# Performance work log

Measured on AMD Instinct MI355X. Metric: run time of the kernel, lower is better.

The kernel has to match this reference:

```python
import jax, jax.numpy as jnp
import numpy as np

B, D, H = 512, 1024, 2048          # batch, context_dim, l_hidden
MAX_STEPS = 8                       # config.max_l_steps
ATOL = 0.01                         # config.l_conv_atol
THR = 0.1                           # config.commitment_threshold


def setup_inputs() -> dict:
    key = jax.random.key(0)
    ks = jax.random.split(key, 20)
    mat = lambda k, shp, fi: jax.random.normal(k, shp, jnp.float32) / np.float32(np.sqrt(fi))
    inp = dict(
        enc=jax.random.normal(ks[0], (B, D), jnp.float32),
        static_context=jax.random.normal(ks[1], (B, D), jnp.float32),
        # fresh RWKV state: channel 3 (pp, running max-exponent) = -1e30
        l_state=jnp.zeros((B, H, 5), jnp.float32).at[:, :, 3].set(-1e30),
        initial_drift=0.1 * jax.random.normal(ks[2], (B, D), jnp.float32),
        # l_input_proj: Linear(2*D -> H)
        Win=mat(ks[3], (2 * D, H), 2 * D), b_in=jnp.zeros((H,), jnp.float32),
        # context_drift_proj: Linear(H -> D, bias=False)
        Wdrift=mat(ks[4], (H, D), H),
        # l_to_out: Linear(H -> D)
        Wout=mat(ks[5], (H, D), H), b_out=jnp.zeros((D,), jnp.float32),
        # RWKV cell (v4-style) parameters over hidden dim H
        mix_k=jax.random.uniform(ks[6], (H,), jnp.float32),
        mix_v=jax.random.uniform(ks[7], (H,), jnp.float32),
        mix_r=jax.random.uniform(ks[8], (H,), jnp.float32),
        mix_k2=jax.random.uniform(ks[9], (H,), jnp.float32),
        mix_r2=jax.random.uniform(ks[10], (H,), jnp.float32),
        time_decay=0.5 * jax.random.normal(ks[11], (H,), jnp.float32),
        time_first=0.5 * jax.random.normal(ks[12], (H,), jnp.float32),
        Wk=mat(ks[13], (H, H), H), Wv=mat(ks[14], (H, H), H),
        Wr=mat(ks[15], (H, H), H), Wo=mat(ks[16], (H, H), H),
        Wk2=mat(ks[17], (H, H), H), Wv2=mat(ks[18], (H, H), H),
        Wr2=mat(ks[19], (H, H), H),
    )
    return inp


def _forward(enc, static_context, l_state, initial_drift, Win, b_in, Wdrift, Wout, b_out,
             mix_k, mix_v, mix_r, mix_k2, mix_r2, time_decay, time_first,
             Wk, Wv, Wr, Wo, Wk2, Wv2, Wr2):
    def cell(x, state):
        # RWKV-style linear-attention cell. state: [B,H,5] = (x_prev_tm, aa, bb, pp, x_prev_cm)
        xx, aa, bb, pp, cc = (state[..., i] for i in range(5))
        xk = x * mix_k + xx * (1.0 - mix_k)
        xv = x * mix_v + xx * (1.0 - mix_v)
        xr = x * mix_r + xx * (1.0 - mix_r)
        r = jax.nn.sigmoid(xr @ Wr)
        k = xk @ Wk
        v = xv @ Wv
        ww = time_first + k
        q = jnp.maximum(pp, ww)
        e1 = jnp.exp(pp - q); e2 = jnp.exp(ww - q)
        wkv = (e1 * aa + e2 * v) / (e1 * bb + e2)
        ww2 = pp - jnp.exp(time_decay)
        q2 = jnp.maximum(ww2, k)
        e1b = jnp.exp(ww2 - q2); e2b = jnp.exp(k - q2)
        tm_out = (r * wkv) @ Wo
        # channel-mix half of the cell (state channel 4)
        xk2 = x * mix_k2 + cc * (1.0 - mix_k2)
        xr2 = x * mix_r2 + cc * (1.0 - mix_r2)
        r2 = jax.nn.sigmoid(xr2 @ Wr2)
        kk = jnp.square(jax.nn.relu(xk2 @ Wk2))
        out = tm_out + r2 * (kk @ Wv2)
        new_state = jnp.stack([x, e1b * aa + e2b * v, e1b * bb + e2b, q2, x], axis=-1)
        return out, new_state

    def l_input_of(drift):
        v = jnp.concatenate([enc, static_context + drift], axis=-1) @ Win + b_in
        return jnp.clip(v, -50.0, 50.0)

    def step(carry, _):
        drift, sstate, done, csum, cnt = carry
        li = l_input_of(drift)
        out, ns = cell(li, sstate)
        ns = jnp.clip(ns, -50.0, 50.0)
        delta = jnp.tanh(out @ Wdrift)
        nd = jnp.clip(drift + delta, -5.0, 5.0)
        hinge = jnp.minimum(jax.nn.relu(jnp.mean(jnp.sum(nd * nd, axis=-1)) - THR), 100.0)
        conv = jnp.mean(jnp.abs(delta)) < ATOL
        # freeze all updates once converged (early-exit semantics under jit)
        drift = jnp.where(done, drift, nd)
        sstate = jnp.where(done, sstate, ns)
        csum = jnp.where(done, csum, csum + hinge)
        cnt = jnp.where(done, cnt, cnt + 1.0)
        done = jnp.logical_or(done, conv)
        return (drift, sstate, done, csum, cnt), None

    carry0 = (initial_drift, l_state, jnp.array(False), jnp.float32(0.0), jnp.float32(0.0))
    (drift, _, _, csum, cnt), _ = jax.lax.scan(step, carry0, None, length=MAX_STEPS)

    # final commit step uses the ORIGINAL l_state (not the shadow state)
    li = l_input_of(drift)
    final_out, next_state = cell(li, l_state)
    next_state = jnp.clip(next_state, -50.0, 50.0)
    final_enc = enc + final_out @ Wout + b_out
    commitment = csum / jnp.maximum(cnt, 1.0)
    return final_enc, next_state, commitment, drift


def reference(enc, static_context, l_state, initial_drift, Win, b_in, Wdrift, Wout, b_out,
              mix_k, mix_v, mix_r, mix_k2, mix_r2, time_decay, time_first,
              Wk, Wv, Wr, Wo, Wk2, Wv2, Wr2):
    return _forward(enc, static_context, l_state, initial_drift, Win, b_in, Wdrift, Wout, b_out,
                    mix_k, mix_v, mix_r, mix_k2, mix_r2, time_decay, time_first,
                    Wk, Wv, Wr, Wo, Wk2, Wv2, Wr2)
```

## Files before the change

### kernel.cpp

```cpp
#include <hip/hip_runtime.h>
#include <hip/hip_bf16.h>

#define Bb 512
#define Dd 1024
#define Hh 2048
#define BH_ (Bb*Hh)
#define BD_ (Bb*Dd)

typedef unsigned short u16;
typedef __attribute__((ext_vector_type(8))) short short8;
typedef __attribute__((ext_vector_type(4))) float f32x4;

enum { M_F32 = 0, M_IN, M_SIG, M_SQRELU, M_OUT, M_DRIFT, M_FINAL };

struct GemmP {
    const u16* A[3];
    const u16* W[3];
    void* dst[3];
    int mode[3];
    int M, N, K;
    const int* done;
    const float* bias;
    const float* mk; const float* mv; const float* mr; const float* mk2v; const float* mr2v;
    const float* xx; const float* cc;
    const float* lstate;
    float* liF;
    float* stateOut;
    u16 *o1, *o2, *o3, *o4, *o5;
    const float* f1; const float* f2;
    float* drift; float* accAbs; float* accSq;
    const float* enc; const float* bout; float* dout;
};

__global__ __launch_bounds__(256) void gemm64(GemmP p) {
    if (p.done && *(volatile const int*)p.done) return;
    const int z = blockIdx.z;
    const u16* __restrict__ A = p.A[z];
    const u16* __restrict__ W = p.W[z];
    const int Kd = p.K;
    const int m0 = blockIdx.y * 64, n0 = blockIdx.x * 64;

    __shared__ alignas(16) u16 As[64 * 72];
    __shared__ alignas(16) u16 Bs[64 * 72];

    const int t = threadIdx.x;
    const int l = t & 63, w = t >> 6;
    const int lane16 = l & 15, quad = l >> 4;
    const int wm = w & 1, wn = w >> 1;
    const int srow = t >> 3, scol = (t & 7) * 8;

    f32x4 zero = {0.f, 0.f, 0.f, 0.f};
    f32x4 acc[2][2];
    acc[0][0] = zero; acc[0][1] = zero; acc[1][0] = zero; acc[1][1] = zero;

    const u16* a0p = A + (size_t)(m0 + srow) * Kd + scol;
    const u16* a1p = A + (size_t)(m0 + srow + 32) * Kd + scol;
    const u16* b0p = W + (size_t)(n0 + srow) * Kd + scol;
    const u16* b1p = W + (size_t)(n0 + srow + 32) * Kd + scol;

    uint4 ra0 = *(const uint4*)(const void*)a0p;
    uint4 ra1 = *(const uint4*)(const void*)a1p;
    uint4 rb0 = *(const uint4*)(const void*)b0p;
    uint4 rb1 = *(const uint4*)(const void*)b1p;

    for (int k0 = 0; k0 < Kd; k0 += 64) {
        *(uint4*)(void*)&As[srow * 72 + scol] = ra0;
        *(uint4*)(void*)&As[(srow + 32) * 72 + scol] = ra1;
        *(uint4*)(void*)&Bs[srow * 72 + scol] = rb0;
        *(uint4*)(void*)&Bs[(srow + 32) * 72 + scol] = rb1;
        __syncthreads();
        if (k0 + 64 < Kd) {
            ra0 = *(const uint4*)(const void*)(a0p + k0 + 64);
            ra1 = *(const uint4*)(const void*)(a1p + k0 + 64);
            rb0 = *(const uint4*)(const void*)(b0p + k0 + 64);
            rb1 = *(const uint4*)(const void*)(b1p + k0 + 64);
        }
#pragma unroll
        for (int kc = 0; kc < 64; kc += 32) {
            short8 a0 = *(const short8*)(const void*)&As[(wm * 32 + lane16) * 72 + kc + quad * 8];
            short8 a1 = *(const short8*)(const void*)&As[(wm * 32 + 16 + lane16) * 72 + kc + quad * 8];
            short8 b0 = *(const short8*)(const void*)&Bs[(wn * 32 + lane16) * 72 + kc + quad * 8];
            short8 b1 = *(const short8*)(const void*)&Bs[(wn * 32 + 16 + lane16) * 72 + kc + quad * 8];
            acc[0][0] = __builtin_amdgcn_mfma_f32_16x16x32_bf16(a0, b0, acc[0][0], 0, 0, 0);
            acc[0][1] = __builtin_amdgcn_mfma_f32_16x16x32_bf16(a0, b1, acc[0][1], 0, 0, 0);
            acc[1][0] = __builtin_amdgcn_mfma_f32_16x16x32_bf16(a1, b0, acc[1][0], 0, 0, 0);
            acc[1][1] = __builtin_amdgcn_mfma_f32_16x16x32_bf16(a1, b1, acc[1][1], 0, 0, 0);
        }
        __syncthreads();
    }

    const int mode = p.mode[z];
    float sabs = 0.f, ssq = 0.f;
#pragma unroll
    for (int sm = 0; sm < 2; ++sm)
#pragma unroll
        for (int sn = 0; sn < 2; ++sn)
#pragma unroll
            for (int i = 0; i < 4; ++i) {
                const int m = m0 + wm * 32 + sm * 16 + quad * 4 + i;
                const int n = n0 + wn * 32 + sn * 16 + lane16;
                const size_t idx = (size_t)m * p.N + n;
                const float v = acc[sm][sn][i];
                if (mode == M_F32) {
                    ((float*)p.dst[z])[idx] = v;
                } else if (mode == M_IN) {
                    float li = fminf(fmaxf(v + p.bias[n], -50.f), 50.f);
                    float xxv, ccv;
                    if (p.lstate) { xxv = p.lstate[idx * 5 + 0]; ccv = p.lstate[idx * 5 + 4]; }
                    else { xxv = p.xx[idx]; ccv = p.cc[idx]; }
                    float mk = p.mk[n], mv = p.mv[n], mr = p.mr[n], mk2 = p.mk2v[n], mr2 = p.mr2v[n];
                    ((__hip_bfloat16*)p.o1)[idx] = __float2bfloat16(li * mk + xxv * (1.f - mk));
                    ((__hip_bfloat16*)p.o2)[idx] = __float2bfloat16(li * mv + xxv * (1.f - mv));
                    ((__hip_bfloat16*)p.o3)[idx] = __float2bfloat16(li * mr + xxv * (1.f - mr));
                    ((__hip_bfloat16*)p.o4)[idx] = __float2bfloat16(li * mk2 + ccv * (1.f - mk2));
                    ((__hip_bfloat16*)p.o5)[idx] = __float2bfloat16(li * mr2 + ccv * (1.f - mr2));
                    if (p.lstate) { p.stateOut[idx * 5 + 0] = li; p.stateOut[idx * 5 + 4] = li; }
                    else p.liF[idx] = li;
                } else if (mode == M_SIG) {
                    ((float*)p.dst[z])[idx] = 1.f / (1.f + __expf(-v));
                } else if (mode == M_SQRELU) {
                    float r = fmaxf(v, 0.f);
                    ((__hip_bfloat16*)p.dst[z])[idx] = __float2bfloat16(r * r);
                } else if (mode == M_OUT) {
                    ((__hip_bfloat16*)p.dst[z])[idx] = __float2bfloat16(p.f1[idx] + p.f2[idx] * v);
                } else if (mode == M_DRIFT) {
                    float d = tanhf(v);
                    float nd = fminf(fmaxf(p.drift[idx] + d, -5.f), 5.f);
                    p.drift[idx] = nd;
                    sabs += fabsf(d);
                    ssq += nd * nd;
                } else {
                    p.dout[idx] = p.enc[idx] + v + p.bout[n];
                }
            }
    if (mode == M_DRIFT) {
#pragma unroll
        for (int off = 32; off > 0; off >>= 1) {
            sabs += __shfl_down(sabs, off, 64);
            ssq += __shfl_down(ssq, off, 64);
        }
        if (l == 0) { atomicAdd(p.accAbs, sabs); atomicAdd(p.accSq, ssq); }
    }
}

__global__ void transposeW(const float* __restrict__ src, u16* __restrict__ dst, int K, int N) {
    __shared__ float tile[32][33];
    int kt = blockIdx.y * 32, nt = blockIdx.x * 32;
    int tx = threadIdx.x, ty = threadIdx.y;
#pragma unroll
    for (int j = 0; j < 4; j++)
        tile[ty + j * 8][tx] = src[(size_t)(kt + ty + j * 8) * N + nt + tx];
    __syncthreads();
    __hip_bfloat16* d = (__hip_bfloat16*)dst;
#pragma unroll
    for (int j = 0; j < 4; j++)
        d[(size_t)(nt + ty + j * 8) * K + kt + tx] = __float2bfloat16(tile[tx][ty + j * 8]);
}

__global__ void initstate(const float* __restrict__ lstate, const float* __restrict__ idrift,
                          float* xx, float* aa, float* bb, float* pp, float* cc,
                          float* drift, float* scal) {
    int i = blockIdx.x * 256 + threadIdx.x;
    if (i < BH_) {
        const float* s = lstate + (size_t)i * 5;
        xx[i] = s[0]; aa[i] = s[1]; bb[i] = s[2]; pp[i] = s[3]; cc[i] = s[4];
    }
    if (i < BD_) drift[i] = idrift[i];
    if (i == 0) { ((int*)scal)[0] = 0; scal[1] = 0.f; scal[2] = 0.f; scal[3] = 0.f; scal[4] = 0.f; }
}

__global__ void prep(const float* __restrict__ enc, const float* __restrict__ sc,
                     const float* __restrict__ drift, u16* __restrict__ Acat, const int* done) {
    if (done && *(volatile const int*)done) return;
    int i = blockIdx.x * 256 + threadIdx.x;
    if (i >= BD_) return;
    int m = i >> 10, d = i & 1023;
    __hip_bfloat16* Ab = (__hip_bfloat16*)Acat;
    Ab[(size_t)m * 2048 + d] = __float2bfloat16(enc[i]);
    Ab[(size_t)m * 2048 + 1024 + d] = __float2bfloat16(sc[i] + drift[i]);
}

__global__ void mix1(const float* __restrict__ Kp, const float* __restrict__ Vp,
                     const float* __restrict__ Rp,
                     float* aa, float* bb, float* pp, float* xx, float* cc,
                     const float* __restrict__ Li,
                     const float* __restrict__ tf, const float* __restrict__ td,
                     u16* __restrict__ rwkv,
                     const float* __restrict__ lstate, float* stateOut,
                     const int* done) {
    if (done && *(volatile const int*)done) return;
    int i = blockIdx.x * 256 + threadIdx.x;
    if (i >= BH_) return;
    int h = i & (Hh - 1);
    float k = Kp[i], v = Vp[i], rpre = Rp[i];
    float a, b, P;
    if (lstate) { a = lstate[(size_t)i * 5 + 1]; b = lstate[(size_t)i * 5 + 2]; P = lstate[(size_t)i * 5 + 3]; }
    else { a = aa[i]; b = bb[i]; P = pp[i]; }
    float r = 1.f / (1.f + __expf(-rpre));
    float ww = tf[h] + k;
    float q = fmaxf(P, ww);
    float e1 = __expf(P - q), e2 = __expf(ww - q);
    float wkv = (e1 * a + e2 * v) / (e1 * b + e2);
    ((__hip_bfloat16*)rwkv)[i] = __float2bfloat16(r * wkv);
    float ww2 = P - __expf(td[h]);
    float q2 = fmaxf(ww2, k);
    float e1b = __expf(ww2 - q2), e2b = __expf(k - q2);
    float na = fminf(fmaxf(e1b * a + e2b * v, -50.f), 50.f);
    float nb = fminf(fmaxf(e1b * b + e2b, -50.f), 50.f);
    float nq = fminf(fmaxf(q2, -50.f), 50.f);
    if (lstate) {
        stateOut[(size_t)i * 5 + 1] = na; stateOut[(size_t)i * 5 + 2] = nb; stateOut[(size_t)i * 5 + 3] = nq;
    } else {
        aa[i] = na; bb[i] = nb; pp[i] = nq;
        float li = Li[i];
        xx[i] = li; cc[i] = li;
    }
}

__global__ void stepfin(float* scal) {
    int* done = (int*)scal;
    if (*done) return;
    float hinge = fminf(fmaxf(scal[4] / (float)Bb - 0.1f, 0.f), 100.f);
    scal[1] += hinge;
    scal[2] += 1.f;
    if (scal[3] / (float)BD_ < 0.01f) *done = 1;
    scal[3] = 0.f; scal[4] = 0.f;
}

__global__ void tailk(const float* __restrict__ scal, const float* __restrict__ drift, float* __restrict__ dout) {
    int i = blockIdx.x * 256 + threadIdx.x;
    const size_t OC = (size_t)BD_ + (size_t)5 * BH_;
    if (i == 0) dout[OC] = scal[1] / fmaxf(scal[2], 1.f);
    if (i < BD_) dout[OC + 1 + i] = drift[i];
}

extern "C" void kernel_launch(void* const* d_in, const int* in_sizes, int n_in,
                              void* d_out, int out_size, void* d_ws, size_t ws_size,
                              hipStream_t stream) {
    const float* enc    = (const float*)d_in[0];
    const float* sc     = (const float*)d_in[1];
    const float* lstate = (const float*)d_in[2];
    const float* idrift = (const float*)d_in[3];
    const float* Win    = (const float*)d_in[4];
    const float* b_in   = (const float*)d_in[5];
    const float* Wdrift = (const float*)d_in[6];
    const float* Wout   = (const float*)d_in[7];
    const float* b_out  = (const float*)d_in[8];
    const float* mix_k  = (const float*)d_in[9];
    const float* mix_v  = (const float*)d_in[10];
    const float* mix_r  = (const float*)d_in[11];
    const float* mix_k2 = (const float*)d_in[12];
    const float* mix_r2 = (const float*)d_in[13];
    const float* tdec   = (const float*)d_in[14];
    const float* tfirst = (const float*)d_in[15];
    const float* Wk  = (const float*)d_in[16];
    const float* Wv  = (const float*)d_in[17];
    const float* Wr  = (const float*)d_in[18];
    const float* Wo  = (const float*)d_in[19];
    const float* Wk2 = (const float*)d_in[20];
    const float* Wv2 = (const float*)d_in[21];
    const float* Wr2 = (const float*)d_in[22];
    float* dout = (float*)d_out;

    const size_t BHs = (size_t)Bb * Hh;
    const size_t BDs = (size_t)Bb * Dd;

    const size_t need_f32 = 9 * BHs + BDs + 16;
    const size_t need_u16 = (size_t)2 * Dd * Hh + 7 * (size_t)Hh * Hh + 2 * (size_t)Hh * Dd + 8 * BHs;
    const size_t need_bytes = need_f32 * 4 + need_u16 * 2;
    if (ws_size < need_bytes) return;

    float* f = (float*)d_ws;
    float* xx  = f;
    float* aa  = xx + BHs;
    float* bbp = aa + BHs;
    float* ppp = bbp + BHs;
    float* cc  = ppp + BHs;
    float* Li  = cc + BHs;
    float* Kp  = Li + BHs;
    float* Vp  = Kp + BHs;
    float* Rp  = Vp + BHs;
    float* Tm  = Kp;
    float* R2  = Vp;
    float* drift = Rp + BHs;
    float* scal  = drift + BDs;
    u16* u = (u16*)(scal + 16);
    u16* WinT  = u; u += (size_t)2 * Dd * Hh;
    u16* WkT   = u; u += (size_t)Hh * Hh;
    u16* WvT   = u; u += (size_t)Hh * Hh;
    u16* WrT   = u; u += (size_t)Hh * Hh;
    u16* WoT   = u; u += (size_t)Hh * Hh;
    u16* Wk2T  = u; u += (size_t)Hh * Hh;
    u16* Wv2T  = u; u += (size_t)Hh * Hh;
    u16* Wr2T  = u; u += (size_t)Hh * Hh;
    u16* WdT   = u; u += (size_t)Hh * Dd;
    u16* WoutT = u; u += (size_t)Hh * Dd;
    u16* Acat = u; u += BHs;
    u16* Xk   = u; u += BHs;
    u16* Xv   = u; u += BHs;
    u16* Xr   = u; u += BHs;
    u16* Xk2  = u; u += BHs;
    u16* Xr2  = u; u += BHs;
    u16* Rw   = u; u += BHs;
    u16* Kk   = u; u += BHs;
    u16* Ob   = Acat;

    int* doneptr = (int*)scal;
    float* accAbs = scal + 3;
    float* accSq  = scal + 4;

    dim3 tb(32, 8);
    transposeW<<<dim3(Hh / 32, (2 * Dd) / 32), tb, 0, stream>>>(Win, WinT, 2 * Dd, Hh);
    transposeW<<<dim3(Hh / 32, Hh / 32), tb, 0, stream>>>(Wk,  WkT,  Hh, Hh);
    transposeW<<<dim3(Hh / 32, Hh / 32), tb, 0, stream>>>(Wv,  WvT,  Hh, Hh);
    transposeW<<<dim3(Hh / 32, Hh / 32), tb, 0, stream>>>(Wr,  WrT,  Hh, Hh);
    transposeW<<<dim3(Hh / 32, Hh / 32), tb, 0, stream>>>(Wo,  WoT,  Hh, Hh);
    transposeW<<<dim3(Hh / 32, Hh / 32), tb, 0, stream>>>(Wk2, Wk2T, Hh, Hh);
    transposeW<<<dim3(Hh / 32, Hh / 32), tb, 0, stream>>>(Wv2, Wv2T, Hh, Hh);
    transposeW<<<dim3(Hh / 32, Hh / 32), tb, 0, stream>>>(Wr2, Wr2T, Hh, Hh);
    transposeW<<<dim3(Dd / 32, Hh / 32), tb, 0, stream>>>(Wdrift, WdT, Hh, Dd);
    transposeW<<<dim3(Dd / 32, Hh / 32), tb, 0, stream>>>(Wout, WoutT, Hh, Dd);

    initstate<<<(BH_ + 255) / 256, 256, 0, stream>>>(lstate, idrift, xx, aa, bbp, ppp, cc, drift, scal);

    GemmP p1 = {};
    p1.A[0] = Acat; p1.W[0] = WinT; p1.mode[0] = M_IN;
    p1.M = Bb; p1.N = Hh; p1.K = 2 * Dd;
    p1.done = doneptr;
    p1.bias = b_in; p1.mk = mix_k; p1.mv = mix_v; p1.mr = mix_r; p1.mk2v = mix_k2; p1.mr2v = mix_r2;
    p1.xx = xx; p1.cc = cc; p1.liF = Li;
    p1.o1 = Xk; p1.o2 = Xv; p1.o3 = Xr; p1.o4 = Xk2; p1.o5 = Xr2;

    GemmP p2 = {};
    p2.A[0] = Xk; p2.A[1] = Xv; p2.A[2] = Xr;
    p2.W[0] = WkT; p2.W[1] = WvT; p2.W[2] = WrT;
    p2.mode[0] = M_F32; p2.mode[1] = M_F32; p2.mode[2] = M_F32;
    p2.dst[0] = Kp; p2.dst[1] = Vp; p2.dst[2] = Rp;
    p2.M = Bb; p2.N = Hh; p2.K = Hh;
    p2.done = doneptr;

    GemmP p3 = {};
    p3.A[0] = Rw; p3.A[1] = Xr2; p3.A[2] = Xk2;
    p3.W[0] = WoT; p3.W[1] = Wr2T; p3.W[2] = Wk2T;
    p3.mode[0] = M_F32; p3.mode[1] = M_SIG; p3.mode[2] = M_SQRELU;
    p3.dst[0] = Tm; p3.dst[1] = R2; p3.dst[2] = Kk;
    p3.M = Bb; p3.N = Hh; p3.K = Hh;
    p3.done = doneptr;

    GemmP p4 = {};
    p4.A[0] = Kk; p4.W[0] = Wv2T; p4.mode[0] = M_OUT; p4.dst[0] = Ob;
    p4.M = Bb; p4.N = Hh; p4.K = Hh;
    p4.f1 = Tm; p4.f2 = R2;
    p4.done = doneptr;

    GemmP p5 = {};
    p5.A[0] = Ob; p5.W[0] = WdT; p5.mode[0] = M_DRIFT;
    p5.M = Bb; p5.N = Dd; p5.K = Hh;
    p5.drift = drift; p5.accAbs = accAbs; p5.accSq = accSq;
    p5.done = doneptr;

    dim3 gH(Hh / 64, Bb / 64, 1);
    dim3 gH3(Hh / 64, Bb / 64, 3);
    dim3 gD(Dd / 64, Bb / 64, 1);

    for (int s = 0; s < 8; ++s) {
        prep<<<(BD_ + 255) / 256, 256, 0, stream>>>(enc, sc, drift, Acat, doneptr);
        gemm64<<<gH, 256, 0, stream>>>(p1);
        gemm64<<<gH3, 256, 0, stream>>>(p2);
        mix1<<<(BH_ + 255) / 256, 256, 0, stream>>>(Kp, Vp, Rp, aa, bbp, ppp, xx, cc, Li,
                                                    tfirst, tdec, Rw, nullptr, nullptr, doneptr);
        gemm64<<<gH3, 256, 0, stream>>>(p3);
        gemm64<<<gH, 256, 0, stream>>>(p4);
        gemm64<<<gD, 256, 0, stream>>>(p5);
        stepfin<<<1, 1, 0, stream>>>(scal);
    }

    float* stateOut = dout + BD_;

    prep<<<(BD_ + 255) / 256, 256, 0, stream>>>(enc, sc, drift, Acat, nullptr);

    GemmP f1p = p1;
    f1p.done = nullptr; f1p.lstate = lstate; f1p.stateOut = stateOut;
    gemm64<<<gH, 256, 0, stream>>>(f1p);

    GemmP f2p = p2; f2p.done = nullptr;
    gemm64<<<gH3, 256, 0, stream>>>(f2p);

    mix1<<<(BH_ + 255) / 256, 256, 0, stream>>>(Kp, Vp, Rp, aa, bbp, ppp, xx, cc, Li,
                                                tfirst, tdec, Rw, lstate, stateOut, nullptr);

    GemmP f3p = p3; f3p.done = nullptr;
    gemm64<<<gH3, 256, 0, stream>>>(f3p);

    GemmP f4p = p4; f4p.done = nullptr;
    gemm64<<<gH, 256, 0, stream>>>(f4p);

    GemmP f5p = {};
    f5p.A[0] = Ob; f5p.W[0] = WoutT; f5p.mode[0] = M_FINAL;
    f5p.M = Bb; f5p.N = Dd; f5p.K = Hh;
    f5p.enc = enc; f5p.bout = b_out; f5p.dout = dout;
    gemm64<<<gD, 256, 0, stream>>>(f5p);

    tailk<<<(BD_ + 255) / 256, 256, 0, stream>>>(scal, drift, dout);
}
```

Before: 1.954 ms.

## Use 128x128 GEMM tiles with direct global-to-LDS loads and fuse step finalization

The GEMM kernel now uses 128x128 output tiles with 4x4 MFMA accumulators per wave instead of 64x64. Operands are copied straight into a swizzled LDS layout with global_load_lds, dropping the padded layout and the register-staged prefetch. The per-step scalar finalization kernel is folded into the drift GEMM: the last block to take an atomic ticket does the hinge and convergence update. The larger tiles cut the grid to 64 blocks for N=2048 and 32 for N=1024, which may leave most CUs idle. The loads are no longer overlapped with compute.

New measurement: 3.425 ms. 1.75x slower.

```diff
diff --git a/kernel.cpp b/kernel.cpp
--- a/kernel.cpp
+++ b/kernel.cpp
@@ -12,6 +12,10 @@
 typedef __attribute__((ext_vector_type(4))) float f32x4;
 
 enum { M_F32 = 0, M_IN, M_SIG, M_SQRELU, M_OUT, M_DRIFT, M_FINAL };
+
+#define GLL(gp, lp) __builtin_amdgcn_global_load_lds( \
+    (const __attribute__((address_space(1))) void*)(gp), \
+    (__attribute__((address_space(3))) void*)(lp), 16, 0, 0)
 
 struct GemmP {
     const u16* A[3];
@@ -29,76 +33,77 @@
     u16 *o1, *o2, *o3, *o4, *o5;
     const float* f1; const float* f2;
     float* drift; float* accAbs; float* accSq;
+    float* scal; int nticket;
     const float* enc; const float* bout; float* dout;
 };
 
-__global__ __launch_bounds__(256) void gemm64(GemmP p) {
+__global__ __launch_bounds__(256) void gemm128(GemmP p) {
     if (p.done && *(volatile const int*)p.done) return;
     const int z = blockIdx.z;
     const u16* __restrict__ A = p.A[z];
     const u16* __restrict__ W = p.W[z];
     const int Kd = p.K;
-    const int m0 = blockIdx.y * 64, n0 = blockIdx.x * 64;
-
-    __shared__ alignas(16) u16 As[64 * 72];
-    __shared__ alignas(16) u16 Bs[64 * 72];
+    const int m0 = blockIdx.y * 128, n0 = blockIdx.x * 128;
+
+    __shared__ alignas(16) u16 As[128 * 64];
+    __shared__ alignas(16) u16 Bs[128 * 64];
 
     const int t = threadIdx.x;
     const int l = t & 63, w = t >> 6;
     const int lane16 = l & 15, quad = l >> 4;
     const int wm = w & 1, wn = w >> 1;
-    const int srow = t >> 3, scol = (t & 7) * 8;
+    const int srow = t >> 3;
+    const int spos = t & 7;
 
     f32x4 zero = {0.f, 0.f, 0.f, 0.f};
-    f32x4 acc[2][2];
-    acc[0][0] = zero; acc[0][1] = zero; acc[1][0] = zero; acc[1][1] = zero;
-
-    const u16* a0p = A + (size_t)(m0 + srow) * Kd + scol;
-    const u16* a1p = A + (size_t)(m0 + srow + 32) * Kd + scol;
-    const u16* b0p = W + (size_t)(n0 + srow) * Kd + scol;
-    const u16* b1p = W + (size_t)(n0 + srow + 32) * Kd + scol;
-
-    uint4 ra0 = *(const uint4*)(const void*)a0p;
-    uint4 ra1 = *(const uint4*)(const void*)a1p;
-    uint4 rb0 = *(const uint4*)(const void*)b0p;
-    uint4 rb1 = *(const uint4*)(const void*)b1p;
+    f32x4 acc[4][4];
+#pragma unroll
+    for (int i = 0; i < 4; ++i)
+#pragma unroll
+        for (int j = 0; j < 4; ++j) acc[i][j] = zero;
 
     for (int k0 = 0; k0 < Kd; k0 += 64) {
-        *(uint4*)(void*)&As[srow * 72 + scol] = ra0;
-        *(uint4*)(void*)&As[(srow + 32) * 72 + scol] = ra1;
-        *(uint4*)(void*)&Bs[srow * 72 + scol] = rb0;
-        *(uint4*)(void*)&Bs[(srow + 32) * 72 + scol] = rb1;
-        __syncthreads();
-        if (k0 + 64 < Kd) {
-            ra0 = *(const uint4*)(const void*)(a0p + k0 + 64);
-            ra1 = *(const uint4*)(const void*)(a1p + k0 + 64);
-            rb0 = *(const uint4*)(const void*)(b0p + k0 + 64);
-            rb1 = *(const uint4*)(const void*)(b1p + k0 + 64);
-        }
-#pragma unroll
-        for (int kc = 0; kc < 64; kc += 32) {
-            short8 a0 = *(const short8*)(const void*)&As[(wm * 32 + lane16) * 72 + kc + quad * 8];
-            short8 a1 = *(const short8*)(const void*)&As[(wm * 32 + 16 + lane16) * 72 + kc + quad * 8];
-            short8 b0 = *(const short8*)(const void*)&Bs[(wn * 32 + lane16) * 72 + kc + quad * 8];
-            short8 b1 = *(const short8*)(const void*)&Bs[(wn * 32 + 16 + lane16) * 72 + kc + quad * 8];
-            acc[0][0] = __builtin_amdgcn_mfma_f32_16x16x32_bf16(a0, b0, acc[0][0], 0, 0, 0);
-            acc[0][1] = __builtin_amdgcn_mfma_f32_16x16x32_bf16(a0, b1, acc[0][1], 0, 0, 0);
-            acc[1][0] = __builtin_amdgcn_mfma_f32_16x16x32_bf16(a1, b0, acc[1][0], 0, 0, 0);
-            acc[1][1] = __builtin_amdgcn_mfma_f32_16x16x32_bf16(a1, b1, acc[1][1], 0, 0, 0);
+#pragma unroll
+        for (int j = 0; j < 4; ++j) {
+            const int r = j * 32 + srow;
+            const int ch = spos ^ (r & 7);
+            GLL(A + (size_t)(m0 + r) * Kd + k0 + ch * 8, &As[r * 64 + spos * 8]);
+            GLL(W + (size_t)(n0 + r) * Kd + k0 + ch * 8, &Bs[r * 64 + spos * 8]);
         }
         __syncthreads();
+#pragma unroll
+        for (int kc = 0; kc < 64; kc += 32) {
+            short8 af[4], bf[4];
+            const int chb = (kc >> 3) + quad;
+#pragma unroll
+            for (int sm = 0; sm < 4; ++sm) {
+                const int r = wm * 64 + sm * 16 + lane16;
+                af[sm] = *(const short8*)(const void*)&As[r * 64 + (chb ^ (r & 7)) * 8];
+            }
+#pragma unroll
+            for (int sn = 0; sn < 4; ++sn) {
+                const int r = wn * 64 + sn * 16 + lane16;
+                bf[sn] = *(const short8*)(const void*)&Bs[r * 64 + (chb ^ (r & 7)) * 8];
+            }
+#pragma unroll
+            for (int sm = 0; sm < 4; ++sm)
+#pragma unroll
+                for (int sn = 0; sn < 4; ++sn)
+                    acc[sm][sn] = __builtin_amdgcn_mfma_f32_16x16x32_bf16(af[sm], bf[sn], acc[sm][sn], 0, 0, 0);
+        }
+        __syncthreads();
     }
 
     const int mode = p.mode[z];
     float sabs = 0.f, ssq = 0.f;
 #pragma unroll
-    for (int sm = 0; sm < 2; ++sm)
-#pragma unroll
-        for (int sn = 0; sn < 2; ++sn)
+    for (int sm = 0; sm < 4; ++sm)
+#pragma unroll
+        for (int sn = 0; sn < 4; ++sn)
 #pragma unroll
             for (int i = 0; i < 4; ++i) {
-                const int m = m0 + wm * 32 + sm * 16 + quad * 4 + i;
-                const int n = n0 + wn * 32 + sn * 16 + lane16;
+                const int m = m0 + wm * 64 + sm * 16 + quad * 4 + i;
+                const int n = n0 + wn * 64 + sn * 16 + lane16;
                 const size_t idx = (size_t)m * p.N + n;
                 const float v = acc[sm][sn][i];
                 if (mode == M_F32) {
@@ -140,6 +145,20 @@
             ssq += __shfl_down(ssq, off, 64);
         }
         if (l == 0) { atomicAdd(p.accAbs, sabs); atomicAdd(p.accSq, ssq); }
+        __syncthreads();
+        if (t == 0) {
+            __threadfence();
+            int v = atomicAdd((int*)(p.scal + 5), 1);
+            if (v == p.nticket - 1) {
+                volatile float* s = p.scal;
+                float hinge = fminf(fmaxf(s[4] / (float)Bb - 0.1f, 0.f), 100.f);
+                s[1] = s[1] + hinge;
+                s[2] = s[2] + 1.f;
+                if (s[3] / (float)BD_ < 0.01f) ((volatile int*)p.scal)[0] = 1;
+                s[3] = 0.f; s[4] = 0.f;
+                ((volatile int*)p.scal)[5] = 0;
+            }
+        }
     }
 }
 
@@ -166,7 +185,10 @@
         xx[i] = s[0]; aa[i] = s[1]; bb[i] = s[2]; pp[i] = s[3]; cc[i] = s[4];
     }
     if (i < BD_) drift[i] = idrift[i];
-    if (i == 0) { ((int*)scal)[0] = 0; scal[1] = 0.f; scal[2] = 0.f; scal[3] = 0.f; scal[4] = 0.f; }
+    if (i == 0) {
+        ((int*)scal)[0] = 0; scal[1] = 0.f; scal[2] = 0.f; scal[3] = 0.f; scal[4] = 0.f;
+        ((int*)scal)[5] = 0;
+    }
 }
 
 __global__ void prep(const float* __restrict__ enc, const float* __restrict__ sc,
@@ -217,16 +239,6 @@
     }
 }
 
-__global__ void stepfin(float* scal) {
-    int* done = (int*)scal;
-    if (*done) return;
-    float hinge = fminf(fmaxf(scal[4] / (float)Bb - 0.1f, 0.f), 100.f);
-    scal[1] += hinge;
-    scal[2] += 1.f;
-    if (scal[3] / (float)BD_ < 0.01f) *done = 1;
-    scal[3] = 0.f; scal[4] = 0.f;
-}
-
 __global__ void tailk(const float* __restrict__ scal, const float* __restrict__ drift, float* __restrict__ dout) {
     int i = blockIdx.x * 256 + threadIdx.x;
     const size_t OC = (size_t)BD_ + (size_t)5 * BH_;
@@ -357,22 +369,22 @@
     p5.A[0] = Ob; p5.W[0] = WdT; p5.mode[0] = M_DRIFT;
     p5.M = Bb; p5.N = Dd; p5.K = Hh;
     p5.drift = drift; p5.accAbs = accAbs; p5.accSq = accSq;
+    p5.scal = scal; p5.nticket = (Dd / 128) * (Bb / 128);
     p5.done = doneptr;
 
-    dim3 gH(Hh / 64, Bb / 64, 1);
-    dim3 gH3(Hh / 64, Bb / 64, 3);
-    dim3 gD(Dd / 64, Bb / 64, 1);
+    dim3 gH(Hh / 128, Bb / 128, 1);
+    dim3 gH3(Hh / 128, Bb / 128, 3);
+    dim3 gD(Dd / 128, Bb / 128, 1);
 
     for (int s = 0; s < 8; ++s) {
         prep<<<(BD_ + 255) / 256, 256, 0, stream>>>(enc, sc, drift, Acat, doneptr);
-        gemm64<<<gH, 256, 0, stream>>>(p1);
-        gemm64<<<gH3, 256, 0, stream>>>(p2);
+        gemm128<<<gH, 256, 0, stream>>>(p1);
+        gemm128<<<gH3, 256, 0, stream>>>(p2);
         mix1<<<(BH_ + 255) / 256, 256, 0, stream>>>(Kp, Vp, Rp, aa, bbp, ppp, xx, cc, Li,
                                                     tfirst, tdec, Rw, nullptr, nullptr, doneptr);
-        gemm64<<<gH3, 256, 0, stream>>>(p3);
-        gemm64<<<gH, 256, 0, stream>>>(p4);
-        gemm64<<<gD, 256, 0, stream>>>(p5);
-        stepfin<<<1, 1, 0, stream>>>(scal);
+        gemm128<<<gH3, 256, 0, stream>>>(p3);
+        gemm128<<<gH, 256, 0, stream>>>(p4);
+        gemm128<<<gD, 256, 0, stream>>>(p5);
     }
 
     float* stateOut = dout + BD_;
@@ -381,25 +393,25 @@
 
     GemmP f1p = p1;
     f1p.done = nullptr; f1p.lstate = lstate; f1p.stateOut = stateOut;
-    gemm64<<<gH, 256, 0, stream>>>(f1p);
+    gemm128<<<gH, 256, 0, stream>>>(f1p);
 
     GemmP f2p = p2; f2p.done = nullptr;
-    gemm64<<<gH3, 256, 0, stream>>>(f2p);
+    gemm128<<<gH3, 256, 0, stream>>>(f2p);
 
     mix1<<<(BH_ + 255) / 256, 256, 0, stream>>>(Kp, Vp, Rp, aa, bbp, ppp, xx, cc, Li,
                                                 tfirst, tdec, Rw, lstate, stateOut, nullptr);
 
     GemmP f3p = p3; f3p.done = nullptr;
-    gemm64<<<gH3, 256, 0, stream>>>(f3p);
+    gemm128<<<gH3, 256, 0, stream>>>(f3p);
 
     GemmP f4p = p4; f4p.done = nullptr;
-    gemm64<<<gH, 256, 0, stream>>>(f4p);
+    gemm128<<<gH, 256, 0, stream>>>(f4p);
 
     GemmP f5p = {};
     f5p.A[0] = Ob; f5p.W[0] = WoutT; f5p.mode[0] = M_FINAL;
     f5p.M = Bb; f5p.N = Dd; f5p.K = Hh;
     f5p.enc = enc; f5p.bout = b_out; f5p.dout = dout;
-    gemm64<<<gD, 256, 0, stream>>>(f5p);
+    gemm128<<<gD, 256, 0, stream>>>(f5p);
 
     tailk<<<(BD_ + 255) / 256, 256, 0, stream>>>(scal, drift, dout);
 }
```
